# Optimization experiments

Measured on AMD Instinct MI355X. Metric: run time of the kernel, lower is better.

The kernel has to match this reference:

```python
import jax, jax.numpy as jnp
import numpy as np

N_NODES = 50000
N_EDGES = 800000
D = 128
N_LAYERS = 3  # n_layers=2 -> 3 attention layers


def setup_inputs() -> dict:
    key = jax.random.key(0)
    ks = jax.random.split(key, 7)
    x = jax.random.normal(ks[0], (N_NODES, D), dtype=jnp.float32)
    edge_src = jax.random.randint(ks[1], (N_EDGES,), 0, N_NODES)
    edge_dst = jax.random.randint(ks[2], (N_EDGES,), 0, N_NODES)
    # Linear weights stored as [in, out] (equivalent to torch W.T)
    lin_w = jax.random.normal(ks[3], (N_LAYERS, D, D), dtype=jnp.float32) / np.sqrt(D)
    lin_b = jax.random.normal(ks[4], (N_LAYERS, D), dtype=jnp.float32) * 0.01
    attn_w = jax.random.normal(ks[5], (N_LAYERS, 2 * D), dtype=jnp.float32) / np.sqrt(2 * D)
    attn_b = jax.random.normal(ks[6], (N_LAYERS,), dtype=jnp.float32) * 0.01
    return {"x": x, "edge_src": edge_src, "edge_dst": edge_dst,
            "lin_w": lin_w, "lin_b": lin_b, "attn_w": attn_w, "attn_b": attn_b}


def reference(x, edge_src, edge_dst, lin_w, lin_b, attn_w, attn_b):
    n = x.shape[0]
    h = x
    for l in range(N_LAYERS):
        # h = leaky_relu(linear(x), 0.2)
        h = jax.nn.leaky_relu(h @ lin_w[l] + lin_b[l], negative_slope=0.2)
        f = h.shape[1]
        # e_ij = attn(cat(h_i, h_j)) -> split the attn weight into left/right halves
        s_left = h @ attn_w[l, :f]   # [N]
        s_right = h @ attn_w[l, f:]  # [N]
        e = s_left[edge_src] + s_right[edge_dst] + attn_b[l]  # [E]
        # sparse softmax over dim=1: normalize per source row i
        m = jax.ops.segment_max(e, edge_src, num_segments=n)
        ex = jnp.exp(e - m[edge_src])
        denom = jax.ops.segment_sum(ex, edge_src, num_segments=n)
        alpha = ex / denom[edge_src]  # [E]
        # h2[i] += h[j] * alpha_ij
        h2 = jax.ops.segment_sum(h[edge_dst] * alpha[:, None], edge_src, num_segments=n)
        h = jax.nn.relu(h2)  # self.activation
    return h
```

## Files before the change

### kernel.cpp

```cpp
#include <hip/hip_runtime.h>
#include <math.h>

#define N_NODES 50000
#define N_EDGES 800000
#define D 128
#define N_LAYERS 3

#define FCHUNK 4096
#define NCHUNK ((N_EDGES + FCHUNK - 1) / FCHUNK)
#define GDIV 6250
#define SLOT 96
#define PREPB ((N_LAYERS * D * D) / 256)
#define CNTB ((N_NODES + 255) / 256)
#define LINB ((N_NODES + 63) / 64)

typedef _Float16 half8 __attribute__((ext_vector_type(8)));
typedef _Float16 half4 __attribute__((ext_vector_type(4)));
typedef float f32x4 __attribute__((ext_vector_type(4)));

__global__ __launch_bounds__(256) void prep_kernel(
    const float* __restrict__ W, _Float16* __restrict__ Wt, int* __restrict__ cnt)
{
    if (blockIdx.x < PREPB) {
        int idx = blockIdx.x * 256 + threadIdx.x;
        int l = idx >> 14, rem = idx & (D * D - 1);
        int k = rem >> 7, n = rem & 127;
        Wt[l * D * D + n * D + k] = (_Float16)W[idx];
    } else {
        int i = (blockIdx.x - PREPB) * 256 + threadIdx.x;
        if (i < N_NODES) cnt[i] = 0;
    }
}

template <bool F32IN, bool FUSEFILL>
__global__ __launch_bounds__(256, 6) void linear_mfma_kernel(
    const void* __restrict__ Ain, const _Float16* __restrict__ Wt,
    const float* __restrict__ b, const float* __restrict__ awr,
    _Float16* __restrict__ hout, float* __restrict__ sr,
    const int* __restrict__ esrc, const int* __restrict__ edst,
    int* __restrict__ cnt, unsigned short* __restrict__ csr16)
{
    __shared__ _Float16 Wl[64 * 130];

    if (FUSEFILL && blockIdx.x >= LINB) {
        int g = blockIdx.x & 7;
        int base = ((blockIdx.x - LINB) >> 3) * FCHUNK;
        int ecnt = N_EDGES - base;
        if (ecnt > FCHUNK) ecnt = FCHUNK;
        unsigned glo = (unsigned)(g * GDIV);
        for (int i = threadIdx.x * 4; i < ecnt; i += 1024) {
            int4 s4 = *(const int4*)(esrc + base + i);
            int4 d4 = *(const int4*)(edst + base + i);
            int ss[4] = {s4.x, s4.y, s4.z, s4.w};
            int dd[4] = {d4.x, d4.y, d4.z, d4.w};
#pragma unroll
            for (int j = 0; j < 4; ++j) {
                if ((unsigned)ss[j] - glo < (unsigned)GDIV) {
                    int pos = atomicAdd(cnt + ss[j], 1);
                    if (pos < SLOT)
                        csr16[(size_t)ss[j] * SLOT + pos] = (unsigned short)dd[j];
                }
            }
        }
        return;
    }

    int tid = threadIdx.x;
    int wid = tid >> 6, lane = tid & 63;
    int m = lane & 15, q = lane >> 4;
    int rowbase = blockIdx.x * 64 + wid * 16;
    int row = rowbase + m;

    half8 a[4];
    if (row < N_NODES) {
        if (F32IN) {
            const float* ar = (const float*)Ain + (size_t)row * D;
#pragma unroll
            for (int s = 0; s < 4; ++s) {
                float4 lo = *(const float4*)(ar + s * 32 + q * 8);
                float4 hi = *(const float4*)(ar + s * 32 + q * 8 + 4);
                a[s][0] = (_Float16)lo.x; a[s][1] = (_Float16)lo.y;
                a[s][2] = (_Float16)lo.z; a[s][3] = (_Float16)lo.w;
                a[s][4] = (_Float16)hi.x; a[s][5] = (_Float16)hi.y;
                a[s][6] = (_Float16)hi.z; a[s][7] = (_Float16)hi.w;
            }
        } else {
            const _Float16* ar = (const _Float16*)Ain + (size_t)row * D;
#pragma unroll
            for (int s = 0; s < 4; ++s)
                a[s] = *(const half8*)(ar + s * 32 + q * 8);
        }
    } else {
#pragma unroll
        for (int s = 0; s < 4; ++s)
#pragma unroll
            for (int j = 0; j < 8; ++j) a[s][j] = (_Float16)0.f;
    }

    f32x4 acc[8];
#pragma unroll
    for (int t = 0; t < 8; ++t) acc[t] = (f32x4)(0.f);

#pragma unroll
    for (int hh = 0; hh < 2; ++hh) {
        for (int j = tid * 8; j < 64 * D; j += 2048) {
            int n = j >> 7, k = j & 127;
            *(half8*)(&Wl[n * 130 + k]) = *(const half8*)(Wt + (hh * 64 + n) * D + k);
        }
        __syncthreads();
#pragma unroll
        for (int s = 0; s < 4; ++s) {
#pragma unroll
            for (int t = 0; t < 4; ++t) {
                half8 bf = *(const half8*)(&Wl[(t * 16 + m) * 130 + s * 32 + q * 8]);
                acc[hh * 4 + t] = __builtin_amdgcn_mfma_f32_16x16x32_f16(a[s], bf, acc[hh * 4 + t], 0, 0, 0);
            }
        }
        __syncthreads();
    }

    float sp[4] = {0.f, 0.f, 0.f, 0.f};
#pragma unroll
    for (int t = 0; t < 8; ++t) {
        int col = t * 16 + m;
        float bc = b[col];
        float ac = awr[col];
#pragma unroll
        for (int r = 0; r < 4; ++r) {
            int orow = rowbase + q * 4 + r;
            float v = acc[t][r] + bc;
            v = v > 0.f ? v : 0.2f * v;
            sp[r] = fmaf(v, ac, sp[r]);
            if (orow < N_NODES)
                hout[(size_t)orow * D + col] = (_Float16)v;
        }
    }
#pragma unroll
    for (int r = 0; r < 4; ++r) {
#pragma unroll
        for (int o = 1; o < 16; o <<= 1)
            sp[r] += __shfl_xor(sp[r], o, 64);
    }
    if (m == 0) {
#pragma unroll
        for (int r = 0; r < 4; ++r) {
            int orow = rowbase + q * 4 + r;
            if (orow < N_NODES) sr[orow] = sp[r];
        }
    }
}

__global__ __launch_bounds__(256, 8) void gather_kernel(
    const int* __restrict__ cnt, const unsigned short* __restrict__ csr16,
    const float* __restrict__ sr, const _Float16* __restrict__ h,
    _Float16* __restrict__ out16, float* __restrict__ out32)
{
    __shared__ int plds[4][2 * SLOT + 8];
    int wid = threadIdx.x >> 6, lane = threadIdx.x & 63;
    int r = lane >> 4, c = lane & 15;
    int n = blockIdx.x * 4 + wid;
    int deg = cnt[n];
    if (deg > SLOT) deg = SLOT;
    const unsigned short* ce = csr16 + (size_t)n * SLOT;
    int* prow = plds[wid];

    float ev[2];
    float m = -INFINITY;
#pragma unroll
    for (int t = 0; t < 2; ++t) {
        int k = t * 64 + lane;
        if (k < deg) {
            int d = ce[k];
            prow[2 * k] = d << 8;
            float e = sr[d];
            ev[t] = e;
            m = fmaxf(m, e);
        }
    }
    for (int o = 32; o > 0; o >>= 1) m = fmaxf(m, __shfl_xor(m, o, 64));

    float s = 0.f;
#pragma unroll
    for (int t = 0; t < 2; ++t) {
        int k = t * 64 + lane;
        if (k < deg) {
            float a = __expf(ev[t] - m);
            prow[2 * k + 1] = __float_as_int(a);
            s += a;
        }
    }
    for (int o = 32; o > 0; o >>= 1) s += __shfl_xor(s, o, 64);
    float inv = (deg > 0) ? 1.f / s : 0.f;

    float acc[8];
#pragma unroll
    for (int j = 0; j < 8; ++j) acc[j] = 0.f;
    const char* hb = (const char*)h + c * 16;

    int k = 0;
    int degU = deg & ~15;
    for (; k < degU; k += 16) {
        int2 p0 = *(const int2*)(prow + 2 * (k + r));
        int2 p1 = *(const int2*)(prow + 2 * (k + 4 + r));
        int2 p2 = *(const int2*)(prow + 2 * (k + 8 + r));
        int2 p3 = *(const int2*)(prow + 2 * (k + 12 + r));
        half8 h0 = *(const half8*)(hb + p0.x);
        half8 h1 = *(const half8*)(hb + p1.x);
        half8 h2 = *(const half8*)(hb + p2.x);
        half8 h3 = *(const half8*)(hb + p3.x);
        float a0 = __int_as_float(p0.y);
        float a1 = __int_as_float(p1.y);
        float a2 = __int_as_float(p2.y);
        float a3 = __int_as_float(p3.y);
#pragma unroll
        for (int j = 0; j < 8; ++j) acc[j] = fmaf((float)h0[j], a0, acc[j]);
#pragma unroll
        for (int j = 0; j < 8; ++j) acc[j] = fmaf((float)h1[j], a1, acc[j]);
#pragma unroll
        for (int j = 0; j < 8; ++j) acc[j] = fmaf((float)h2[j], a2, acc[j]);
#pragma unroll
        for (int j = 0; j < 8; ++j) acc[j] = fmaf((float)h3[j], a3, acc[j]);
    }
    for (; k < deg; k += 4) {
        int kk = k + r;
        int2 p = (kk < deg) ? *(const int2*)(prow + 2 * kk) : make_int2(0, 0);
        half8 hv = *(const half8*)(hb + p.x);
        float a = __int_as_float(p.y);
#pragma unroll
        for (int j = 0; j < 8; ++j) acc[j] = fmaf((float)hv[j], a, acc[j]);
    }

#pragma unroll
    for (int j = 0; j < 8; ++j) {
        acc[j] += __shfl_xor(acc[j], 16, 64);
        acc[j] += __shfl_xor(acc[j], 32, 64);
    }

    if (r == 0) {
        float rv[8];
#pragma unroll
        for (int j = 0; j < 8; ++j) rv[j] = fmaxf(acc[j] * inv, 0.f);
        if (out16) {
            half8 o;
#pragma unroll
            for (int j = 0; j < 8; ++j) o[j] = (_Float16)rv[j];
            *(half8*)(out16 + (size_t)n * D + c * 8) = o;
        } else {
            float4 lo = make_float4(rv[0], rv[1], rv[2], rv[3]);
            float4 hi = make_float4(rv[4], rv[5], rv[6], rv[7]);
            *(float4*)(out32 + (size_t)n * D + c * 8) = lo;
            *(float4*)(out32 + (size_t)n * D + c * 8 + 4) = hi;
        }
    }
}

extern "C" void kernel_launch(void* const* d_in, const int* in_sizes, int n_in,
                              void* d_out, int out_size, void* d_ws, size_t ws_size,
                              hipStream_t stream)
{
    const float* x      = (const float*)d_in[0];
    const int*   esrc   = (const int*)d_in[1];
    const int*   edst   = (const int*)d_in[2];
    const float* lin_w  = (const float*)d_in[3];
    const float* lin_b  = (const float*)d_in[4];
    const float* attn_w = (const float*)d_in[5];
    float* out = (float*)d_out;

    char* ws = (char*)d_ws;
    _Float16*       h16A  = (_Float16*)(ws);
    _Float16*       h16B  = (_Float16*)(ws + 12800000);
    float*          sr    = (float*)(ws + 25600000);
    int*            cnt   = (int*)(ws + 25800000);
    unsigned short* csr16 = (unsigned short*)(ws + 26000000);
    _Float16*       Wt16  = (_Float16*)(ws + 35600000);

    prep_kernel<<<PREPB + CNTB, 256, 0, stream>>>(lin_w, Wt16, cnt);

    for (int l = 0; l < N_LAYERS; ++l) {
        bool last = (l == N_LAYERS - 1);
        if (l == 0)
            linear_mfma_kernel<true, true><<<LINB + NCHUNK * 8, 256, 0, stream>>>(
                x, Wt16, lin_b, attn_w + D, h16A, sr,
                esrc, edst, cnt, csr16);
        else
            linear_mfma_kernel<false, false><<<LINB, 256, 0, stream>>>(
                h16B, Wt16 + (size_t)l * D * D, lin_b + (size_t)l * D,
                attn_w + (size_t)l * 2 * D + D, h16A, sr,
                nullptr, nullptr, nullptr, nullptr);
        gather_kernel<<<N_NODES / 4, 256, 0, stream>>>(
            cnt, csr16, sr, h16A,
            last ? (_Float16*)nullptr : h16B, last ? out : nullptr);
    }
}
```

Measured before the change: 258.7 us.

## Split per-node CSR fill into 8 sub-buckets to cut atomic contention

Edge bucketing now uses 8 per-node sub-counters, chosen by fill block index, each with 16 slots of pre-shifted int offsets. The old fill had 8 blocks per chunk each rescanning the chunk for a node range; now each 1024-edge block processes its edges once. The gather kernel rebuilds a compact neighbor list with an 8-lane prefix scan over the sub-counts. This removes redundant edge rereads and spreads atomics across counters, but it raises CSR memory and can drop edges if more than 16 land in one sub-bucket.

Result: slower. 288.0 us (+11.4%).

```diff
diff --git a/kernel.cpp b/kernel.cpp
--- a/kernel.cpp
+++ b/kernel.cpp
@@ -6,12 +6,13 @@
 #define D 128
 #define N_LAYERS 3
 
-#define FCHUNK 4096
+#define FCHUNK 1024
 #define NCHUNK ((N_EDGES + FCHUNK - 1) / FCHUNK)
-#define GDIV 6250
-#define SLOT 96
+#define GROUPS 8
+#define GSLOT 16
+#define ROWSLOT (GROUPS * GSLOT)
 #define PREPB ((N_LAYERS * D * D) / 256)
-#define CNTB ((N_NODES + 255) / 256)
+#define CNT8B ((N_NODES * GROUPS + 255) / 256)
 #define LINB ((N_NODES + 63) / 64)
 
 typedef _Float16 half8 __attribute__((ext_vector_type(8)));
@@ -19,7 +20,7 @@
 typedef float f32x4 __attribute__((ext_vector_type(4)));
 
 __global__ __launch_bounds__(256) void prep_kernel(
-    const float* __restrict__ W, _Float16* __restrict__ Wt, int* __restrict__ cnt)
+    const float* __restrict__ W, _Float16* __restrict__ Wt, int* __restrict__ cnt8)
 {
     if (blockIdx.x < PREPB) {
         int idx = blockIdx.x * 256 + threadIdx.x;
@@ -28,7 +29,7 @@
         Wt[l * D * D + n * D + k] = (_Float16)W[idx];
     } else {
         int i = (blockIdx.x - PREPB) * 256 + threadIdx.x;
-        if (i < N_NODES) cnt[i] = 0;
+        if (i < N_NODES * GROUPS) cnt8[i] = 0;
     }
 }
 
@@ -38,29 +39,29 @@
     const float* __restrict__ b, const float* __restrict__ awr,
     _Float16* __restrict__ hout, float* __restrict__ sr,
     const int* __restrict__ esrc, const int* __restrict__ edst,
-    int* __restrict__ cnt, unsigned short* __restrict__ csr16)
+    int* __restrict__ cnt8, int* __restrict__ csr32)
 {
     __shared__ _Float16 Wl[64 * 130];
 
     if (FUSEFILL && blockIdx.x >= LINB) {
-        int g = blockIdx.x & 7;
-        int base = ((blockIdx.x - LINB) >> 3) * FCHUNK;
+        int fi = blockIdx.x - LINB;
+        int g = fi & 7;
+        int base = fi * FCHUNK;
         int ecnt = N_EDGES - base;
         if (ecnt > FCHUNK) ecnt = FCHUNK;
-        unsigned glo = (unsigned)(g * GDIV);
-        for (int i = threadIdx.x * 4; i < ecnt; i += 1024) {
+        int i = threadIdx.x * 4;
+        if (i < ecnt) {
             int4 s4 = *(const int4*)(esrc + base + i);
             int4 d4 = *(const int4*)(edst + base + i);
-            int ss[4] = {s4.x, s4.y, s4.z, s4.w};
-            int dd[4] = {d4.x, d4.y, d4.z, d4.w};
-#pragma unroll
-            for (int j = 0; j < 4; ++j) {
-                if ((unsigned)ss[j] - glo < (unsigned)GDIV) {
-                    int pos = atomicAdd(cnt + ss[j], 1);
-                    if (pos < SLOT)
-                        csr16[(size_t)ss[j] * SLOT + pos] = (unsigned short)dd[j];
-                }
-            }
+            int pos;
+            pos = atomicAdd(cnt8 + s4.x * GROUPS + g, 1);
+            if (pos < GSLOT) csr32[(size_t)s4.x * ROWSLOT + g * GSLOT + pos] = d4.x << 8;
+            pos = atomicAdd(cnt8 + s4.y * GROUPS + g, 1);
+            if (pos < GSLOT) csr32[(size_t)s4.y * ROWSLOT + g * GSLOT + pos] = d4.y << 8;
+            pos = atomicAdd(cnt8 + s4.z * GROUPS + g, 1);
+            if (pos < GSLOT) csr32[(size_t)s4.z * ROWSLOT + g * GSLOT + pos] = d4.z << 8;
+            pos = atomicAdd(cnt8 + s4.w * GROUPS + g, 1);
+            if (pos < GSLOT) csr32[(size_t)s4.w * ROWSLOT + g * GSLOT + pos] = d4.w << 8;
         }
         return;
     }
@@ -151,28 +152,40 @@
 }
 
 __global__ __launch_bounds__(256, 8) void gather_kernel(
-    const int* __restrict__ cnt, const unsigned short* __restrict__ csr16,
+    const int* __restrict__ cnt8, const int* __restrict__ csr32,
     const float* __restrict__ sr, const _Float16* __restrict__ h,
     _Float16* __restrict__ out16, float* __restrict__ out32)
 {
-    __shared__ int plds[4][2 * SLOT + 8];
+    __shared__ int plds[4][2 * ROWSLOT + 8];
     int wid = threadIdx.x >> 6, lane = threadIdx.x & 63;
     int r = lane >> 4, c = lane & 15;
     int n = blockIdx.x * 4 + wid;
-    int deg = cnt[n];
-    if (deg > SLOT) deg = SLOT;
-    const unsigned short* ce = csr16 + (size_t)n * SLOT;
     int* prow = plds[wid];
+
+    int myc = cnt8[n * GROUPS + (lane & 7)];
+    myc = myc > GSLOT ? GSLOT : myc;
+    int p = myc;
+#pragma unroll
+    for (int o = 1; o < 8; o <<= 1) {
+        int u = __shfl_up(p, o, 8);
+        if ((lane & 7) >= o) p += u;
+    }
+    int excl = p - myc;
+    int deg = __shfl(p, 7, 8);
+    int gl = lane >> 3;
+    int cg = __shfl(myc, gl, 8);
+    int pg = __shfl(excl, gl, 8);
+    const int* ce = csr32 + (size_t)n * ROWSLOT + gl * GSLOT;
 
     float ev[2];
     float m = -INFINITY;
 #pragma unroll
     for (int t = 0; t < 2; ++t) {
-        int k = t * 64 + lane;
-        if (k < deg) {
-            int d = ce[k];
-            prow[2 * k] = d << 8;
-            float e = sr[d];
+        int j = (lane & 7) + t * 8;
+        if (j < cg) {
+            int dofs = ce[j];
+            prow[2 * (pg + j)] = dofs;
+            float e = sr[dofs >> 8];
             ev[t] = e;
             m = fmaxf(m, e);
         }
@@ -182,10 +195,10 @@
     float s = 0.f;
 #pragma unroll
     for (int t = 0; t < 2; ++t) {
-        int k = t * 64 + lane;
-        if (k < deg) {
+        int j = (lane & 7) + t * 8;
+        if (j < cg) {
             float a = __expf(ev[t] - m);
-            prow[2 * k + 1] = __float_as_int(a);
+            prow[2 * (pg + j) + 1] = __float_as_int(a);
             s += a;
         }
     }
@@ -223,9 +236,9 @@
     }
     for (; k < deg; k += 4) {
         int kk = k + r;
-        int2 p = (kk < deg) ? *(const int2*)(prow + 2 * kk) : make_int2(0, 0);
-        half8 hv = *(const half8*)(hb + p.x);
-        float a = __int_as_float(p.y);
+        int2 pp = (kk < deg) ? *(const int2*)(prow + 2 * kk) : make_int2(0, 0);
+        half8 hv = *(const half8*)(hb + pp.x);
+        float a = __int_as_float(pp.y);
 #pragma unroll
         for (int j = 0; j < 8; ++j) acc[j] = fmaf((float)hv[j], a, acc[j]);
     }
@@ -267,28 +280,28 @@
     float* out = (float*)d_out;
 
     char* ws = (char*)d_ws;
-    _Float16*       h16A  = (_Float16*)(ws);
-    _Float16*       h16B  = (_Float16*)(ws + 12800000);
-    float*          sr    = (float*)(ws + 25600000);
-    int*            cnt   = (int*)(ws + 25800000);
-    unsigned short* csr16 = (unsigned short*)(ws + 26000000);
-    _Float16*       Wt16  = (_Float16*)(ws + 35600000);
-
-    prep_kernel<<<PREPB + CNTB, 256, 0, stream>>>(lin_w, Wt16, cnt);
+    _Float16* h16A  = (_Float16*)(ws);
+    _Float16* h16B  = (_Float16*)(ws + 12800000);
+    float*    sr    = (float*)(ws + 25600000);
+    int*      cnt8  = (int*)(ws + 25800000);
+    int*      csr32 = (int*)(ws + 27400000);
+    _Float16* Wt16  = (_Float16*)(ws + 53000000);
+
+    prep_kernel<<<PREPB + CNT8B, 256, 0, stream>>>(lin_w, Wt16, cnt8);
 
     for (int l = 0; l < N_LAYERS; ++l) {
         bool last = (l == N_LAYERS - 1);
         if (l == 0)
-            linear_mfma_kernel<true, true><<<LINB + NCHUNK * 8, 256, 0, stream>>>(
+            linear_mfma_kernel<true, true><<<LINB + NCHUNK, 256, 0, stream>>>(
                 x, Wt16, lin_b, attn_w + D, h16A, sr,
-                esrc, edst, cnt, csr16);
+                esrc, edst, cnt8, csr32);
         else
             linear_mfma_kernel<false, false><<<LINB, 256, 0, stream>>>(
                 h16B, Wt16 + (size_t)l * D * D, lin_b + (size_t)l * D,
                 attn_w + (size_t)l * 2 * D + D, h16A, sr,
                 nullptr, nullptr, nullptr, nullptr);
         gather_kernel<<<N_NODES / 4, 256, 0, stream>>>(
-            cnt, csr16, sr, h16A,
+            cnt8, csr32, sr, h16A,
             last ? (_Float16*)nullptr : h16B, last ? out : nullptr);
     }
 }
```
